# Performance work log

Hardware: AMD Instinct MI355X
Metric: run time of the kernel (lower is better)

Reference implementation:

```python
import jax, jax.numpy as jnp
import numpy as np

N = 4096
DK = 128   # d_k == d_e == d_h (required by gate shapes in KAG)
DH = 128
DR = 64
DE = 128
NHEADS = 3
ALPHA = 0.2
NEG_INF = -9e15


def _xavier(k, shape, gain=1.414):
    fan_in, fan_out = shape[-2], shape[-1]
    limit = gain * np.sqrt(6.0 / (fan_in + fan_out))
    return jax.random.uniform(k, shape, minval=-limit, maxval=limit, dtype=jnp.float32)


def setup_inputs() -> dict:
    key = jax.random.key(0)
    ks = jax.random.split(key, 16)
    x = jax.random.normal(ks[0], (N, DK), dtype=jnp.float32)
    adj = (jax.random.uniform(ks[1], (N, N)) < 0.01).astype(jnp.float32)
    adj = jnp.maximum(adj, jnp.eye(N, dtype=jnp.float32))
    e_t = jax.random.normal(ks[2], (N, DE), dtype=jnp.float32)
    r_t = jax.random.normal(ks[3], (N, DR), dtype=jnp.float32)
    prev_h = jax.random.normal(ks[4], (N, DH), dtype=jnp.float32)
    # GAT params: NHEADS input heads + one output head
    W_heads = _xavier(ks[5], (NHEADS, DK, DH))
    a_heads = _xavier(ks[6], (NHEADS, 2 * DH, 1))
    W_out = _xavier(ks[7], (NHEADS * DH, DH))
    a_out = _xavier(ks[8], (2 * DH, 1))
    # KAG + OutputLayer linear params (stored [in, out])
    din_kag = DK + DR + DH  # 320
    Wq_w = _xavier(ks[9], (din_kag, DK), gain=1.0)
    Wq_b = jnp.zeros((DK,), jnp.float32)
    Wh_w = _xavier(ks[10], (din_kag, DH), gain=1.0)
    Wh_b = jnp.zeros((DH,), jnp.float32)
    din_out = DK + DE + DH  # 384
    Wp_w = _xavier(ks[11], (din_out, DH), gain=1.0)
    Wp_b = jnp.zeros((DH,), jnp.float32)
    return {"x": x, "adj": adj, "e_t": e_t, "r_t": r_t, "prev_h": prev_h,
            "W_heads": W_heads, "a_heads": a_heads, "W_out": W_out, "a_out": a_out,
            "Wq_w": Wq_w, "Wq_b": Wq_b, "Wh_w": Wh_w, "Wh_b": Wh_b,
            "Wp_w": Wp_w, "Wp_b": Wp_b}


def _gat_layer(h, adj, W, a, concat):
    # h: [N, Fin], W: [Fin, F], a: [2F, 1]
    Wh = h @ W                       # [N, F]
    F_ = W.shape[1]
    # a^T [Wh_i ; Wh_j] == (Wh a1)_i + (Wh a2)_j  -- identical math, no [N,N,2F]
    f1 = Wh @ a[:F_]                 # [N, 1]
    f2 = Wh @ a[F_:]                 # [N, 1]
    e = jax.nn.leaky_relu(f1 + f2.T, negative_slope=ALPHA)  # [N, N]
    e = jnp.where(adj > 0, e, NEG_INF)
    att = jax.nn.softmax(e, axis=1)  # dropout(p=0.6) is identity in eval mode
    h_prime = att @ Wh               # [N, F]
    return jax.nn.elu(h_prime) if concat else h_prime


def reference(x, adj, e_t, r_t, prev_h, W_heads, a_heads, W_out, a_out,
              Wq_w, Wq_b, Wh_w, Wh_b, Wp_w, Wp_b):
    # --- GAT ---
    heads = jax.vmap(lambda W, a: _gat_layer(x, adj, W, a, True))(W_heads, a_heads)  # [H,N,DH]
    h_cat = jnp.transpose(heads, (1, 0, 2)).reshape(N, NHEADS * DH)
    h_gat = jax.nn.elu(_gat_layer(h_cat, adj, W_out, a_out, False))  # [N, DH]
    # --- KAG gated update (x_t := e_t per CEKT.forward call) ---
    comb = jnp.concatenate([e_t, r_t, prev_h], axis=1)  # [N, DE+DR+DH]
    g = jax.nn.sigmoid(comb @ Wq_w + Wq_b)
    cand = jnp.tanh(comb @ Wh_w + Wh_b)
    h_t = (1.0 - g) * prev_h + g * cand                 # [N, DH]
    # --- Output layer (kc_t := x per CEKT.forward call) ---
    comb2 = jnp.concatenate([h_t, e_t, x], axis=1)      # [N, DH+DE+DK]
    y_t = jax.nn.sigmoid(comb2 @ Wp_w + Wp_b)           # [N, DH]
    return y_t
```

## Files before the change

### kernel.cpp

```cpp
#include <hip/hip_runtime.h>
#include <hip/hip_bf16.h>


typedef short s16x8 __attribute__((ext_vector_type(8)));
typedef float f32x4 __attribute__((ext_vector_type(4)));

constexpr int NKQ = 10;
constexpr int NKP = 12;
constexpr int CH_Q = 0, CH_H = 80, CH_P = 160, NCHUNK = 256;

__device__ __forceinline__ ushort bf16_rne(float f) {
    union { float f; uint u; } a; a.f = f;
    return (ushort)((a.u + 0x7FFFu + ((a.u >> 16) & 1u)) >> 16);
}
__device__ __forceinline__ float bf16_to_f(ushort h) {
    union { uint u; float f; } b; b.u = ((uint)h) << 16;
    return b.f;
}
__device__ __forceinline__ void split2(float f, ushort& hi, ushort& lo) {
    hi = bf16_rne(f);
    lo = bf16_rne(f - bf16_to_f(hi));
}
__device__ __forceinline__ float fsigmoid(float z) {
    return 1.0f / (1.0f + __expf(-z));
}
__device__ __forceinline__ float ftanh(float z) {
    const float a = fabsf(z);
    const float t = __expf(-2.0f * a);
    const float r = (1.0f - t) / (1.0f + t);
    return copysignf(r, z);
}

__global__ __launch_bounds__(128) void prep_w(
    const float* __restrict__ Wq, const float* __restrict__ Wh,
    const float* __restrict__ Wp, ushort* __restrict__ ws)
{
    const int chunk = blockIdx.x;
    const int t = threadIdx.x;
    const int jp = t >> 6, l = t & 63;
    const float* W;
    int s, ct;
    if (chunk < CH_H)      { W = Wq; ct = chunk / NKQ;          s = chunk % NKQ; }
    else if (chunk < CH_P) { W = Wh; ct = (chunk - CH_H) / NKQ; s = (chunk - CH_H) % NKQ; }
    else                   { W = Wp; ct = (chunk - CH_P) / NKP; s = (chunk - CH_P) % NKP; }
    const int col = ct * 16 + (l & 15);
    const int kbase = s * 32 + (l >> 4) * 8 + jp * 4;
    ushort hi[4];
#pragma unroll
    for (int j2 = 0; j2 < 4; ++j2)
        hi[j2] = bf16_rne(W[(kbase + j2) * 128 + col]);
    const int ub = (chunk * 64 + l) * 8 + jp * 4;
    *(uint2*)&ws[ub] = *(const uint2*)hi;
}

__global__ __launch_bounds__(1024, 1) void cekt_mfma(
    const float* __restrict__ x,
    const float* __restrict__ e_t,
    const float* __restrict__ r_t,
    const float* __restrict__ prev_h,
    const float* __restrict__ bq,
    const float* __restrict__ bh,
    const float* __restrict__ bp,
    const ushort* __restrict__ ws,
    float* __restrict__ out)
{
    __shared__ alignas(16) ushort A1h[NKQ * 64 * 8], A1l[NKQ * 64 * 8];
    __shared__ alignas(16) ushort A2h[NKP * 64 * 8];
    __shared__ f32x4 p1g[8][64], p1c[8][64], p2y[8][64];

    const int t = threadIdx.x;
    const int row0 = blockIdx.x * 16;
    const int w = t >> 6, lane = t & 63;
    const int ct = w & 7, kh = w >> 3;

    const s16x8* whv = (const s16x8*)ws;

    for (int i = t; i < 1280; i += 1024) {
        const int row = i / 80, kq4 = i - row * 80;
        const int k0 = kq4 * 4;
        float4 v;
        if (k0 < 128)      v = *(const float4*)&e_t[(row0 + row) * 128 + k0];
        else if (k0 < 192) v = *(const float4*)&r_t[(row0 + row) * 64 + (k0 - 128)];
        else               v = *(const float4*)&prev_h[(row0 + row) * 128 + (k0 - 192)];
        const int s = k0 >> 5, q = (k0 >> 3) & 3, j0 = k0 & 7;
        const int base = (s * 64 + q * 16 + row) * 8 + j0;
        ushort hi4[4], lo4[4];
        split2(v.x, hi4[0], lo4[0]); split2(v.y, hi4[1], lo4[1]);
        split2(v.z, hi4[2], lo4[2]); split2(v.w, hi4[3], lo4[3]);
        *(uint2*)&A1h[base] = *(const uint2*)hi4;
        *(uint2*)&A1l[base] = *(const uint2*)lo4;
    }
    {
        const int row = t >> 6, kr = t & 63;
        const int k0 = 128 + kr * 4;
        const float4 v = (k0 < 256)
            ? *(const float4*)&e_t[(row0 + row) * 128 + (k0 - 128)]
            : *(const float4*)&x[(row0 + row) * 128 + (k0 - 256)];
        const int s = k0 >> 5, q = (k0 >> 3) & 3, j0 = k0 & 7;
        const int base = (s * 64 + q * 16 + row) * 8 + j0;
        ushort hi4[4];
        hi4[0] = bf16_rne(v.x); hi4[1] = bf16_rne(v.y);
        hi4[2] = bf16_rne(v.z); hi4[3] = bf16_rne(v.w);
        *(uint2*)&A2h[base] = *(const uint2*)hi4;
    }

    const int sbeg = kh * 5;
    s16x8 hq[5], hc[5];
#pragma unroll
    for (int si = 0; si < 5; ++si) {
        const int cq = (CH_Q + ct * NKQ + sbeg + si) * 64 + lane;
        const int cc = (CH_H + ct * NKQ + sbeg + si) * 64 + lane;
        hq[si] = whv[cq];
        hc[si] = whv[cc];
    }
    __syncthreads();

    f32x4 gacc = {0, 0, 0, 0}, cacc = {0, 0, 0, 0};
#pragma unroll
    for (int si = 0; si < 5; ++si) {
        const int s = sbeg + si;
        const s16x8 aH = *(const s16x8*)&A1h[(s * 64 + lane) * 8];
        const s16x8 aL = *(const s16x8*)&A1l[(s * 64 + lane) * 8];
        gacc = __builtin_amdgcn_mfma_f32_16x16x32_bf16(aH, hq[si], gacc, 0, 0, 0);
        cacc = __builtin_amdgcn_mfma_f32_16x16x32_bf16(aH, hc[si], cacc, 0, 0, 0);
        gacc = __builtin_amdgcn_mfma_f32_16x16x32_bf16(aL, hq[si], gacc, 0, 0, 0);
        cacc = __builtin_amdgcn_mfma_f32_16x16x32_bf16(aL, hc[si], cacc, 0, 0, 0);
    }

    s16x8 pH[6];
    if (kh) {
        p1g[ct][lane] = gacc;
        p1c[ct][lane] = cacc;
#pragma unroll
        for (int si = 0; si < 6; ++si)
            pH[si] = whv[(CH_P + ct * NKP + 6 + si) * 64 + lane];
    }
    __syncthreads();

    f32x4 yacc = {0, 0, 0, 0};
    s16x8 rH[6];
    if (!kh) {
#pragma unroll
        for (int si = 0; si < 6; ++si)
            rH[si] = whv[(CH_P + ct * NKP + si) * 64 + lane];
        gacc += p1g[ct][lane];
        cacc += p1c[ct][lane];
        const int colL = lane & 15, rg = lane >> 4;
        const int col = ct * 16 + colL;
        const float bqv = bq[col], bhv = bh[col];
        const int s_h = col >> 5, q_h = (col >> 3) & 3, j_h = col & 7;
#pragma unroll
        for (int i2 = 0; i2 < 4; ++i2) {
            const int row = rg * 4 + i2;
            const float ph = prev_h[(row0 + row) * 128 + col];
            const float g = fsigmoid(gacc[i2] + bqv);
            const float cd = ftanh(cacc[i2] + bhv);
            const float h = (1.0f - g) * ph + g * cd;
            const int idx = (s_h * 64 + q_h * 16 + row) * 8 + j_h;
            A2h[idx] = bf16_rne(h);
        }
    } else {
#pragma unroll
        for (int si = 0; si < 6; ++si) {
            const int s = 6 + si;
            const s16x8 aH = *(const s16x8*)&A2h[(s * 64 + lane) * 8];
            yacc = __builtin_amdgcn_mfma_f32_16x16x32_bf16(aH, pH[si], yacc, 0, 0, 0);
        }
        p2y[ct][lane] = yacc;
    }
    __syncthreads();

    if (!kh) {
        yacc = p2y[ct][lane];
#pragma unroll
        for (int si = 0; si < 6; ++si) {
            const s16x8 aH = *(const s16x8*)&A2h[(si * 64 + lane) * 8];
            yacc = __builtin_amdgcn_mfma_f32_16x16x32_bf16(aH, rH[si], yacc, 0, 0, 0);
        }
        const int colL = lane & 15, rg = lane >> 4;
        const int col = ct * 16 + colL;
        const float bpv = bp[col];
#pragma unroll
        for (int i2 = 0; i2 < 4; ++i2) {
            const int row = rg * 4 + i2;
            out[(row0 + row) * 128 + col] = fsigmoid(yacc[i2] + bpv);
        }
    }
}

extern "C" void kernel_launch(void* const* d_in, const int* in_sizes, int n_in,
                              void* d_out, int out_size, void* d_ws, size_t ws_size,
                              hipStream_t stream) {
    const float* x      = (const float*)d_in[0];
    const float* e_t    = (const float*)d_in[2];
    const float* r_t    = (const float*)d_in[3];
    const float* prev_h = (const float*)d_in[4];
    const float* Wq_w   = (const float*)d_in[9];
    const float* Wq_b   = (const float*)d_in[10];
    const float* Wh_w   = (const float*)d_in[11];
    const float* Wh_b   = (const float*)d_in[12];
    const float* Wp_w   = (const float*)d_in[13];
    const float* Wp_b   = (const float*)d_in[14];
    float* out  = (float*)d_out;
    ushort* ws  = (ushort*)d_ws;

    hipLaunchKernelGGL(prep_w, dim3(NCHUNK), dim3(128), 0, stream,
                       Wq_w, Wh_w, Wp_w, ws);
    hipLaunchKernelGGL(cekt_mfma, dim3(256), dim3(1024), 0, stream,
                       x, e_t, r_t, prev_h, Wq_b, Wh_b, Wp_b, ws, out);
}
```

Measured before the change: 16.26 us.

## Halve rows per block, drop split-K reduction, double grid size

Each block now handles 8 rows instead of 16 with 512 threads, and each wave computes the full K range itself, which removes the cross-wave partial-sum exchange through shared memory and one barrier. The unused half of each 16-row MFMA tile is zero-filled in shared memory. The grid doubles to 512 blocks so more CUs are occupied. The cost is that half of every MFMA computes on padding and each block reloads the full weight set, doubling weight traffic per output row.

```diff
diff --git a/kernel.cpp b/kernel.cpp
--- a/kernel.cpp
+++ b/kernel.cpp
@@ -8,6 +8,7 @@
 constexpr int NKQ = 10;
 constexpr int NKP = 12;
 constexpr int CH_Q = 0, CH_H = 80, CH_P = 160, NCHUNK = 256;
+constexpr int BMR = 8;
 
 __device__ __forceinline__ ushort bf16_rne(float f) {
     union { float f; uint u; } a; a.f = f;
@@ -53,7 +54,7 @@
     *(uint2*)&ws[ub] = *(const uint2*)hi;
 }
 
-__global__ __launch_bounds__(1024, 1) void cekt_mfma(
+__global__ __launch_bounds__(512, 2) void cekt_mfma(
     const float* __restrict__ x,
     const float* __restrict__ e_t,
     const float* __restrict__ r_t,
@@ -66,16 +67,30 @@
 {
     __shared__ alignas(16) ushort A1h[NKQ * 64 * 8], A1l[NKQ * 64 * 8];
     __shared__ alignas(16) ushort A2h[NKP * 64 * 8];
-    __shared__ f32x4 p1g[8][64], p1c[8][64], p2y[8][64];
 
     const int t = threadIdx.x;
-    const int row0 = blockIdx.x * 16;
-    const int w = t >> 6, lane = t & 63;
-    const int ct = w & 7, kh = w >> 3;
+    const int row0 = blockIdx.x * BMR;
+    const int ct = t >> 6, lane = t & 63;
 
     const s16x8* whv = (const s16x8*)ws;
 
-    for (int i = t; i < 1280; i += 1024) {
+    for (int i = t; i < 1024; i += 512) {
+        const uint4 z = {0, 0, 0, 0};
+        if (i < 320) {
+            const int c = i >> 3, s = c >> 2, q = c & 3;
+            *(uint4*)&A1h[(s * 64 + q * 16 + 8) * 8 + (i & 7) * 8] = z;
+        } else if (i < 640) {
+            const int i2 = i - 320;
+            const int c = i2 >> 3, s = c >> 2, q = c & 3;
+            *(uint4*)&A1l[(s * 64 + q * 16 + 8) * 8 + (i2 & 7) * 8] = z;
+        } else {
+            const int i2 = i - 640;
+            const int c = i2 >> 3, s = c >> 2, q = c & 3;
+            *(uint4*)&A2h[(s * 64 + q * 16 + 8) * 8 + (i2 & 7) * 8] = z;
+        }
+    }
+
+    for (int i = t; i < 640; i += 512) {
         const int row = i / 80, kq4 = i - row * 80;
         const int k0 = kq4 * 4;
         float4 v;
@@ -104,86 +119,73 @@
         *(uint2*)&A2h[base] = *(const uint2*)hi4;
     }
 
-    const int sbeg = kh * 5;
     s16x8 hq[5], hc[5];
 #pragma unroll
     for (int si = 0; si < 5; ++si) {
-        const int cq = (CH_Q + ct * NKQ + sbeg + si) * 64 + lane;
-        const int cc = (CH_H + ct * NKQ + sbeg + si) * 64 + lane;
-        hq[si] = whv[cq];
-        hc[si] = whv[cc];
+        hq[si] = whv[(CH_Q + ct * NKQ + si) * 64 + lane];
+        hc[si] = whv[(CH_H + ct * NKQ + si) * 64 + lane];
     }
     __syncthreads();
 
     f32x4 gacc = {0, 0, 0, 0}, cacc = {0, 0, 0, 0};
 #pragma unroll
-    for (int si = 0; si < 5; ++si) {
-        const int s = sbeg + si;
+    for (int s = 0; s < NKQ; ++s) {
+        s16x8 q_, c_;
+        if (s < 5) { q_ = hq[s]; c_ = hc[s]; }
+        else {
+            q_ = whv[(CH_Q + ct * NKQ + s) * 64 + lane];
+            c_ = whv[(CH_H + ct * NKQ + s) * 64 + lane];
+        }
         const s16x8 aH = *(const s16x8*)&A1h[(s * 64 + lane) * 8];
         const s16x8 aL = *(const s16x8*)&A1l[(s * 64 + lane) * 8];
-        gacc = __builtin_amdgcn_mfma_f32_16x16x32_bf16(aH, hq[si], gacc, 0, 0, 0);
-        cacc = __builtin_amdgcn_mfma_f32_16x16x32_bf16(aH, hc[si], cacc, 0, 0, 0);
-        gacc = __builtin_amdgcn_mfma_f32_16x16x32_bf16(aL, hq[si], gacc, 0, 0, 0);
-        cacc = __builtin_amdgcn_mfma_f32_16x16x32_bf16(aL, hc[si], cacc, 0, 0, 0);
-    }
-
-    s16x8 pH[6];
-    if (kh) {
-        p1g[ct][lane] = gacc;
-        p1c[ct][lane] = cacc;
-#pragma unroll
-        for (int si = 0; si < 6; ++si)
-            pH[si] = whv[(CH_P + ct * NKP + 6 + si) * 64 + lane];
-    }
-    __syncthreads();
-
-    f32x4 yacc = {0, 0, 0, 0};
+        gacc = __builtin_amdgcn_mfma_f32_16x16x32_bf16(aH, q_, gacc, 0, 0, 0);
+        cacc = __builtin_amdgcn_mfma_f32_16x16x32_bf16(aH, c_, cacc, 0, 0, 0);
+        gacc = __builtin_amdgcn_mfma_f32_16x16x32_bf16(aL, q_, gacc, 0, 0, 0);
+        cacc = __builtin_amdgcn_mfma_f32_16x16x32_bf16(aL, c_, cacc, 0, 0, 0);
+    }
+
     s16x8 rH[6];
-    if (!kh) {
-#pragma unroll
-        for (int si = 0; si < 6; ++si)
-            rH[si] = whv[(CH_P + ct * NKP + si) * 64 + lane];
-        gacc += p1g[ct][lane];
-        cacc += p1c[ct][lane];
+#pragma unroll
+    for (int si = 0; si < 6; ++si)
+        rH[si] = whv[(CH_P + ct * NKP + si) * 64 + lane];
+
+    {
         const int colL = lane & 15, rg = lane >> 4;
         const int col = ct * 16 + colL;
         const float bqv = bq[col], bhv = bh[col];
         const int s_h = col >> 5, q_h = (col >> 3) & 3, j_h = col & 7;
-#pragma unroll
-        for (int i2 = 0; i2 < 4; ++i2) {
-            const int row = rg * 4 + i2;
-            const float ph = prev_h[(row0 + row) * 128 + col];
-            const float g = fsigmoid(gacc[i2] + bqv);
-            const float cd = ftanh(cacc[i2] + bhv);
-            const float h = (1.0f - g) * ph + g * cd;
-            const int idx = (s_h * 64 + q_h * 16 + row) * 8 + j_h;
-            A2h[idx] = bf16_rne(h);
-        }
-    } else {
-#pragma unroll
-        for (int si = 0; si < 6; ++si) {
-            const int s = 6 + si;
-            const s16x8 aH = *(const s16x8*)&A2h[(s * 64 + lane) * 8];
-            yacc = __builtin_amdgcn_mfma_f32_16x16x32_bf16(aH, pH[si], yacc, 0, 0, 0);
-        }
-        p2y[ct][lane] = yacc;
+        if (rg < 2) {
+#pragma unroll
+            for (int i2 = 0; i2 < 4; ++i2) {
+                const int row = rg * 4 + i2;
+                const float ph = prev_h[(row0 + row) * 128 + col];
+                const float g = fsigmoid(gacc[i2] + bqv);
+                const float cd = ftanh(cacc[i2] + bhv);
+                const float h = (1.0f - g) * ph + g * cd;
+                A2h[(s_h * 64 + q_h * 16 + row) * 8 + j_h] = bf16_rne(h);
+            }
+        }
     }
     __syncthreads();
 
-    if (!kh) {
-        yacc = p2y[ct][lane];
-#pragma unroll
-        for (int si = 0; si < 6; ++si) {
-            const s16x8 aH = *(const s16x8*)&A2h[(si * 64 + lane) * 8];
-            yacc = __builtin_amdgcn_mfma_f32_16x16x32_bf16(aH, rH[si], yacc, 0, 0, 0);
-        }
+    f32x4 yacc = {0, 0, 0, 0};
+#pragma unroll
+    for (int s = 0; s < NKP; ++s) {
+        const s16x8 pB = (s < 6) ? rH[s]
+                                 : whv[(CH_P + ct * NKP + s) * 64 + lane];
+        const s16x8 aH = *(const s16x8*)&A2h[(s * 64 + lane) * 8];
+        yacc = __builtin_amdgcn_mfma_f32_16x16x32_bf16(aH, pB, yacc, 0, 0, 0);
+    }
+    {
         const int colL = lane & 15, rg = lane >> 4;
         const int col = ct * 16 + colL;
         const float bpv = bp[col];
-#pragma unroll
-        for (int i2 = 0; i2 < 4; ++i2) {
-            const int row = rg * 4 + i2;
-            out[(row0 + row) * 128 + col] = fsigmoid(yacc[i2] + bpv);
+        if (rg < 2) {
+#pragma unroll
+            for (int i2 = 0; i2 < 4; ++i2) {
+                const int row = rg * 4 + i2;
+                out[(row0 + row) * 128 + col] = fsigmoid(yacc[i2] + bpv);
+            }
         }
     }
 }
@@ -206,6 +208,6 @@
 
     hipLaunchKernelGGL(prep_w, dim3(NCHUNK), dim3(128), 0, stream,
                        Wq_w, Wh_w, Wp_w, ws);
-    hipLaunchKernelGGL(cekt_mfma, dim3(256), dim3(1024), 0, stream,
+    hipLaunchKernelGGL(cekt_mfma, dim3(4096 / BMR), dim3(512), 0, stream,
                        x, e_t, r_t, prev_h, Wq_b, Wh_b, Wp_b, ws, out);
 }
```

Measured after the change: 18.39 us. 1.13x slower.

## Fuse weight bf16 conversion into main kernel, drop prep launch

Applied to the files above, without the earlier changes.

Removes the separate prep_w kernel that converted the weights to bf16 MFMA fragments in a workspace. Each wave now reads fp32 weights straight from global memory and rounds them to bf16 fragments in registers. Weight loads are issued before the activation staging so they can overlap it. This saves one kernel launch and the workspace round trip. In exchange, every block redoes the weight conversion, and the loads are strided 8-element column gathers rather than contiguous 16-byte vectors.

```diff
diff --git a/kernel.cpp b/kernel.cpp
--- a/kernel.cpp
+++ b/kernel.cpp
@@ -7,7 +7,6 @@
 
 constexpr int NKQ = 10;
 constexpr int NKP = 12;
-constexpr int CH_Q = 0, CH_H = 80, CH_P = 160, NCHUNK = 256;
 
 __device__ __forceinline__ ushort bf16_rne(float f) {
     union { float f; uint u; } a; a.f = f;
@@ -31,37 +30,27 @@
     return copysignf(r, z);
 }
 
-__global__ __launch_bounds__(128) void prep_w(
-    const float* __restrict__ Wq, const float* __restrict__ Wh,
-    const float* __restrict__ Wp, ushort* __restrict__ ws)
-{
-    const int chunk = blockIdx.x;
-    const int t = threadIdx.x;
-    const int jp = t >> 6, l = t & 63;
-    const float* W;
-    int s, ct;
-    if (chunk < CH_H)      { W = Wq; ct = chunk / NKQ;          s = chunk % NKQ; }
-    else if (chunk < CH_P) { W = Wh; ct = (chunk - CH_H) / NKQ; s = (chunk - CH_H) % NKQ; }
-    else                   { W = Wp; ct = (chunk - CH_P) / NKP; s = (chunk - CH_P) % NKP; }
-    const int col = ct * 16 + (l & 15);
-    const int kbase = s * 32 + (l >> 4) * 8 + jp * 4;
-    ushort hi[4];
+__device__ __forceinline__ s16x8 ldfrag(const float* __restrict__ W,
+                                        int s, int krow, int colW) {
+    const float* p = W + (s * 32 + krow) * 128 + colW;
+    union { ushort u[8]; s16x8 v; } r;
 #pragma unroll
-    for (int j2 = 0; j2 < 4; ++j2)
-        hi[j2] = bf16_rne(W[(kbase + j2) * 128 + col]);
-    const int ub = (chunk * 64 + l) * 8 + jp * 4;
-    *(uint2*)&ws[ub] = *(const uint2*)hi;
+    for (int j = 0; j < 8; ++j)
+        r.u[j] = bf16_rne(p[j * 128]);
+    return r.v;
 }
 
-__global__ __launch_bounds__(1024, 1) void cekt_mfma(
+__global__ __launch_bounds__(1024, 1) void cekt_fused(
     const float* __restrict__ x,
     const float* __restrict__ e_t,
     const float* __restrict__ r_t,
     const float* __restrict__ prev_h,
+    const float* __restrict__ Wq,
+    const float* __restrict__ Wh,
+    const float* __restrict__ Wp,
     const float* __restrict__ bq,
     const float* __restrict__ bh,
     const float* __restrict__ bp,
-    const ushort* __restrict__ ws,
     float* __restrict__ out)
 {
     __shared__ alignas(16) ushort A1h[NKQ * 64 * 8], A1l[NKQ * 64 * 8];
@@ -72,8 +61,16 @@
     const int row0 = blockIdx.x * 16;
     const int w = t >> 6, lane = t & 63;
     const int ct = w & 7, kh = w >> 3;
+    const int krow = (lane >> 4) * 8;
+    const int colW = ct * 16 + (lane & 15);
 
-    const s16x8* whv = (const s16x8*)ws;
+    const int sbeg = kh * 5;
+    s16x8 hq[5], hc[5];
+#pragma unroll
+    for (int si = 0; si < 5; ++si) {
+        hq[si] = ldfrag(Wq, sbeg + si, krow, colW);
+        hc[si] = ldfrag(Wh, sbeg + si, krow, colW);
+    }
 
     for (int i = t; i < 1280; i += 1024) {
         const int row = i / 80, kq4 = i - row * 80;
@@ -103,16 +100,6 @@
         hi4[2] = bf16_rne(v.z); hi4[3] = bf16_rne(v.w);
         *(uint2*)&A2h[base] = *(const uint2*)hi4;
     }
-
-    const int sbeg = kh * 5;
-    s16x8 hq[5], hc[5];
-#pragma unroll
-    for (int si = 0; si < 5; ++si) {
-        const int cq = (CH_Q + ct * NKQ + sbeg + si) * 64 + lane;
-        const int cc = (CH_H + ct * NKQ + sbeg + si) * 64 + lane;
-        hq[si] = whv[cq];
-        hc[si] = whv[cc];
-    }
     __syncthreads();
 
     f32x4 gacc = {0, 0, 0, 0}, cacc = {0, 0, 0, 0};
@@ -133,7 +120,7 @@
         p1c[ct][lane] = cacc;
 #pragma unroll
         for (int si = 0; si < 6; ++si)
-            pH[si] = whv[(CH_P + ct * NKP + 6 + si) * 64 + lane];
+            pH[si] = ldfrag(Wp, 6 + si, krow, colW);
     }
     __syncthreads();
 
@@ -142,7 +129,7 @@
     if (!kh) {
 #pragma unroll
         for (int si = 0; si < 6; ++si)
-            rH[si] = whv[(CH_P + ct * NKP + si) * 64 + lane];
+            rH[si] = ldfrag(Wp, si, krow, colW);
         gacc += p1g[ct][lane];
         cacc += p1c[ct][lane];
         const int colL = lane & 15, rg = lane >> 4;
@@ -156,8 +143,7 @@
             const float g = fsigmoid(gacc[i2] + bqv);
             const float cd = ftanh(cacc[i2] + bhv);
             const float h = (1.0f - g) * ph + g * cd;
-            const int idx = (s_h * 64 + q_h * 16 + row) * 8 + j_h;
-            A2h[idx] = bf16_rne(h);
+            A2h[(s_h * 64 + q_h * 16 + row) * 8 + j_h] = bf16_rne(h);
         }
     } else {
 #pragma unroll
@@ -202,10 +188,8 @@
     const float* Wp_w   = (const float*)d_in[13];
     const float* Wp_b   = (const float*)d_in[14];
     float* out  = (float*)d_out;
-    ushort* ws  = (ushort*)d_ws;
 
-    hipLaunchKernelGGL(prep_w, dim3(NCHUNK), dim3(128), 0, stream,
-                       Wq_w, Wh_w, Wp_w, ws);
-    hipLaunchKernelGGL(cekt_mfma, dim3(256), dim3(1024), 0, stream,
-                       x, e_t, r_t, prev_h, Wq_b, Wh_b, Wp_b, ws, out);
+    hipLaunchKernelGGL(cekt_fused, dim3(256), dim3(1024), 0, stream,
+                       x, e_t, r_t, prev_h, Wq_w, Wh_w, Wp_w,
+                       Wq_b, Wh_b, Wp_b, out);
 }
```

New measurement: 15.06 us. 7.4% less time.
